# Optimization experiments

Hardware: AMD Instinct MI355X
Metric: run time of the kernel (lower is better)

## Reference

```python
import jax, jax.numpy as jnp
import numpy as np

B, N, C = 128, 197, 768
H = 12
HID = 3072
DROP = 0.1
EPS = 1e-5


def _layernorm(x, g, b):
    m = jnp.mean(x, axis=-1, keepdims=True)
    v = jnp.var(x, axis=-1, keepdims=True)
    return (x - m) * jax.lax.rsqrt(v + EPS) * g + b


def setup_inputs() -> dict:
    key = jax.random.key(0)
    ks = jax.random.split(key, 6)
    def lin(k, fan_in, fan_out):
        return (jax.random.normal(k, (fan_in, fan_out), jnp.float32) * (fan_in ** -0.5))
    return {
        "x": jax.random.normal(ks[0], (B, N, C), jnp.float32),
        "ln1_g": jnp.ones((C,), jnp.float32),
        "ln1_b": jnp.zeros((C,), jnp.float32),
        "Wqkv": lin(ks[1], C, 3 * C),          # qkv_bias=False
        "Wproj": lin(ks[2], C, C),
        "bproj": jnp.zeros((C,), jnp.float32),
        "ln2_g": jnp.ones((C,), jnp.float32),
        "ln2_b": jnp.zeros((C,), jnp.float32),
        "W1": lin(ks[3], C, HID),
        "b1": jnp.zeros((HID,), jnp.float32),
        "W2": lin(ks[4], HID, C),
        "b2": jnp.zeros((C,), jnp.float32),
    }


def reference(x, ln1_g, ln1_b, Wqkv, Wproj, bproj, ln2_g, ln2_b, W1, b1, W2, b2):
    Bx, Nx, Cx = x.shape
    hd = Cx // H
    thr = int((Nx - 1) * DROP)            # 19
    keep = (Nx - 1) - (thr + 1)           # 176 patches kept (rank > thr)

    # ---- drop_low_attn: unscaled q@k^T, mean over heads, cls->patch scores ----
    qkv = (x @ Wqkv).reshape(Bx, Nx, 3, H, hd).transpose(2, 0, 3, 1, 4)
    q, k = qkv[0], qkv[1]
    attn0 = jnp.einsum('bhnd,bhmd->bhnm', q, k)        # no scale, no softmax
    scores = jnp.mean(attn0, axis=1)[:, 0, 1:]          # [B, N-1]
    rank = jnp.argsort(jnp.argsort(scores, axis=1), axis=1)
    keep_mask = rank > thr                              # exactly `keep` True per row
    # indices of kept patches in original order (stable argsort of ~mask)
    idx = jnp.argsort((~keep_mask).astype(jnp.int32), axis=1)[:, :keep] + 1
    tok = jnp.concatenate([jnp.zeros((Bx, 1), idx.dtype), idx], axis=1)  # cls + kept
    x = jnp.take_along_axis(x, tok[:, :, None], axis=1) / (1.0 - DROP)   # [B, 177, C]
    Np = keep + 1

    # ---- attention block (scaled softmax attention) ----
    h = _layernorm(x, ln1_g, ln1_b)
    qkv2 = (h @ Wqkv).reshape(Bx, Np, 3, H, hd).transpose(2, 0, 3, 1, 4)
    q2, k2, v2 = qkv2[0], qkv2[1], qkv2[2]
    a = jax.nn.softmax(jnp.einsum('bhnd,bhmd->bhnm', q2, k2) * (hd ** -0.5), axis=-1)
    o = jnp.einsum('bhnm,bhmd->bhnd', a, v2).transpose(0, 2, 1, 3).reshape(Bx, Np, Cx)
    x = x + (o @ Wproj + bproj)

    # ---- MLP block ----
    h = _layernorm(x, ln2_g, ln2_b)
    x = x + (jax.nn.gelu(h @ W1 + b1, approximate=False) @ W2 + b2)
    return x
```

## Files before the change

kernel.cpp:

```cpp
#include <hip/hip_runtime.h>
#include <math.h>

#define BB 128
#define NTOK 197
#define CC 768
#define HH 12
#define HD 64
#define HIDN 3072
#define NP 177
#define NPATCH 196
#define THRK 19
#define MR (BB*NP)

using short8 = __attribute__((ext_vector_type(8))) short;
using f32x4  = __attribute__((ext_vector_type(4))) float;

__device__ __forceinline__ unsigned short f2b(float f){
  unsigned u = __builtin_bit_cast(unsigned, f);
  u += 0x7fffu + ((u >> 16) & 1u);
  return (unsigned short)(u >> 16);
}

__device__ __forceinline__ float fast_gelu(float v){
  float u = v * 0.70710678118654752f;
  float a = fabsf(u);
  float t = 1.0f / fmaf(0.3275911f, a, 1.0f);
  float p = fmaf(1.061405429f, t, -1.453152027f);
  p = fmaf(p, t, 1.421413741f);
  p = fmaf(p, t, -0.284496736f);
  p = fmaf(p, t, 0.254829592f);
  p = p * t;
  float e = __expf(-a*a);
  float erfu = copysignf(1.0f - p*e, u);
  return 0.5f * v * (1.0f + erfu);
}

__device__ __forceinline__ void gload16(const void* src, void* lds){
  __builtin_amdgcn_global_load_lds(
      (const __attribute__((address_space(1))) unsigned int*)src,
      (__attribute__((address_space(3))) unsigned int*)lds,
      16, 0, 0);
}

__global__ void tcvt_kernel(const float* __restrict__ in, unsigned short* __restrict__ out, int K, int N){
  __shared__ float tile[64][65];
  int n0 = blockIdx.x*64, k0 = blockIdx.y*64;
  int t = threadIdx.x;
  int r = t >> 6, c = t & 63;
  #pragma unroll
  for (int i = 0; i < 16; ++i)
    tile[r + i*4][c] = in[(size_t)(k0 + r + i*4)*N + n0 + c];
  __syncthreads();
  #pragma unroll
  for (int i = 0; i < 16; ++i)
    out[(size_t)(n0 + r + i*4)*K + k0 + c] = f2b(tile[c][r + i*4]);
}

__global__ void q0_kernel(const float* __restrict__ x, const float* __restrict__ Wqkv, float* __restrict__ q0){
  int b = blockIdx.x, t = threadIdx.x;
  int c = blockIdx.y*256 + t;
  __shared__ float xs[CC];
  for (int j = t; j < CC; j += 256) xs[j] = x[(size_t)b*NTOK*CC + j];
  __syncthreads();
  double acc = 0.0;
  for (int j = 0; j < CC; ++j) acc = fma((double)xs[j], (double)Wqkv[(size_t)j*(3*CC) + c], acc);
  q0[b*CC + c] = (float)acc;
}

__global__ void wvec_kernel(const float* __restrict__ Wqkv, const float* __restrict__ q0, float* __restrict__ wv){
  int b = blockIdx.x;
  int j = blockIdx.y*4 + (threadIdx.x >> 6);
  int l = threadIdx.x & 63;
  const float* row = Wqkv + (size_t)j*(3*CC) + CC;
  const float* qs = q0 + b*CC;
  double acc = 0.0;
  for (int c = l; c < CC; c += 64) acc = fma((double)row[c], (double)qs[c], acc);
  for (int off = 32; off; off >>= 1) acc += __shfl_down(acc, off);
  if (l == 0) wv[b*CC + j] = (float)acc;
}

__global__ void score_kernel(const float* __restrict__ x, const float* __restrict__ wv, float* __restrict__ sc){
  int m = blockIdx.x, b = blockIdx.y, l = threadIdx.x;
  const float* xr = x + ((size_t)b*NTOK + 1 + m)*CC;
  const float* wr = wv + b*CC;
  double acc = 0.0;
  for (int c = l; c < CC; c += 64) acc = fma((double)xr[c], (double)wr[c], acc);
  for (int off = 32; off; off >>= 1) acc += __shfl_down(acc, off);
  if (l == 0) sc[b*NPATCH + m] = (float)(acc * (1.0/12.0));
}

__global__ void select_kernel(const float* __restrict__ sc, int* __restrict__ tok){
  int b = blockIdx.x, t = threadIdx.x;
  __shared__ float s[NPATCH];
  __shared__ int kp[NPATCH];
  for (int m = t; m < NPATCH; m += 256) s[m] = sc[b*NPATCH + m];
  __syncthreads();
  for (int m = t; m < NPATCH; m += 256){
    float v = s[m]; int rank = 0;
    for (int j = 0; j < NPATCH; ++j){
      float u = s[j];
      rank += (u < v) || (u == v && j < m);
    }
    kp[m] = (rank > THRK) ? 1 : 0;
  }
  __syncthreads();
  for (int m = t; m < NPATCH; m += 256){
    if (kp[m]){
      int pos = 0;
      for (int j = 0; j < m; ++j) pos += kp[j];
      tok[b*NP + 1 + pos] = m + 1;
    }
  }
  if (t == 0) tok[b*NP] = 0;
}

__global__ void gather_kernel(const float* __restrict__ x, const int* __restrict__ tok, float* __restrict__ xk){
  int i = blockIdx.x, b = blockIdx.y, t = threadIdx.x;
  int src = tok[b*NP + i];
  const float* xr = x + ((size_t)b*NTOK + src)*CC;
  float* o = xk + ((size_t)b*NP + i)*CC;
  for (int c = t; c < CC; c += 256) o[c] = xr[c] * (1.0f/0.9f);
}

__global__ void ln_kernel(const float* __restrict__ in, const float* __restrict__ g,
                          const float* __restrict__ bt, unsigned short* __restrict__ out){
  int row = blockIdx.x, t = threadIdx.x;
  const float* xr = in + (size_t)row*CC;
  float v0 = xr[t], v1 = xr[t+256], v2 = xr[t+512];
  float s = v0+v1+v2, ss = v0*v0+v1*v1+v2*v2;
  for (int off = 32; off; off >>= 1){ s += __shfl_down(s, off); ss += __shfl_down(ss, off); }
  __shared__ float red[8];
  int wid = t >> 6, lane = t & 63;
  if (lane == 0){ red[wid] = s; red[4+wid] = ss; }
  __syncthreads();
  if (t == 0){
    float S = red[0]+red[1]+red[2]+red[3], SS = red[4]+red[5]+red[6]+red[7];
    float mean = S * (1.0f/CC);
    float var = SS * (1.0f/CC) - mean*mean;
    red[0] = mean; red[1] = rsqrtf(var + 1e-5f);
  }
  __syncthreads();
  float mean = red[0], rstd = red[1];
  unsigned short* orow = out + (size_t)row*CC;
  orow[t]     = f2b((v0-mean)*rstd*g[t]     + bt[t]);
  orow[t+256] = f2b((v1-mean)*rstd*g[t+256] + bt[t+256]);
  orow[t+512] = f2b((v2-mean)*rstd*g[t+512] + bt[t+512]);
}

template<int EPI>
__global__ __launch_bounds__(256) void gemm128(
    const unsigned short* __restrict__ A, const unsigned short* __restrict__ Bt,
    const float* __restrict__ bias, const float* __restrict__ res, void* __restrict__ outp,
    int M, int N, int K)
{
  __shared__ __align__(16) short As[2][128*32];
  __shared__ __align__(16) short Bs[2][128*32];
  int nwg = gridDim.x, o = blockIdx.x;
  int q = nwg >> 3, rr = nwg & 7;
  int xcd = o & 7, seq = o >> 3;
  int wg = (xcd < rr) ? xcd*(q+1) + seq : rr*(q+1) + (xcd - rr)*q + seq;
  int nx = N >> 7;
  int m0 = (wg / nx) << 7, n0 = (wg % nx) << 7;

  int t = threadIdx.x, w = t >> 6, l = t & 63;
  int wr = w >> 1, wc = w & 1;
  int srow = w*16 + (l >> 2);
  int sk8  = (l & 3)*8;
  const unsigned short* Abase = A  + (size_t)(m0 + srow)*K + sk8;
  const unsigned short* Bbase = Bt + (size_t)(n0 + srow)*K + sk8;
  f32x4 acc[4][4] = {};

  int nt = K >> 5;
  #pragma unroll
  for (int j = 0; j < 2; ++j){
    gload16(Abase + (size_t)(j*64)*K, &As[0][(j*64 + w*16)*32]);
    gload16(Bbase + (size_t)(j*64)*K, &Bs[0][(j*64 + w*16)*32]);
  }
  __syncthreads();

  int cur = 0;
  for (int ti = 0; ti < nt; ++ti){
    if (ti + 1 < nt){
      int kt = (ti + 1) << 5;
      #pragma unroll
      for (int j = 0; j < 2; ++j){
        gload16(Abase + (size_t)(j*64)*K + kt, &As[cur^1][(j*64 + w*16)*32]);
        gload16(Bbase + (size_t)(j*64)*K + kt, &Bs[cur^1][(j*64 + w*16)*32]);
      }
    }
    short8 af[4], bf[4];
    #pragma unroll
    for (int i = 0; i < 4; ++i){
      af[i] = *reinterpret_cast<const short8*>(&As[cur][(wr*64 + i*16 + (l&15))*32 + (l>>4)*8]);
      bf[i] = *reinterpret_cast<const short8*>(&Bs[cur][(wc*64 + i*16 + (l&15))*32 + (l>>4)*8]);
    }
    #pragma unroll
    for (int i = 0; i < 4; ++i)
      #pragma unroll
      for (int jn = 0; jn < 4; ++jn)
        acc[i][jn] = __builtin_amdgcn_mfma_f32_16x16x32_bf16(af[i], bf[jn], acc[i][jn], 0, 0, 0);
    __syncthreads();
    cur ^= 1;
  }

  #pragma unroll
  for (int i = 0; i < 4; ++i)
  #pragma unroll
  for (int jn = 0; jn < 4; ++jn){
    int row = m0 + wr*64 + i*16 + (l>>4)*4;
    int col = n0 + wc*64 + jn*16 + (l&15);
    #pragma unroll
    for (int r = 0; r < 4; ++r){
      float v = acc[i][jn][r];
      if (EPI != 0) v += bias[col];
      if (EPI == 2) v = fast_gelu(v);
      if (EPI == 1 || EPI == 3) v += res[(size_t)(row+r)*N + col];
      if (EPI == 0 || EPI == 2) ((unsigned short*)outp)[(size_t)(row+r)*N + col] = f2b(v);
      else                      ((float*)outp)[(size_t)(row+r)*N + col] = v;
    }
  }
}

__global__ __launch_bounds__(256) void attn_kernel(const unsigned short* __restrict__ qkv2,
                                                   unsigned short* __restrict__ o)
{
  int rt = blockIdx.x, h = blockIdx.y, b = blockIdx.z;
  int t = threadIdx.x, w = t >> 6, l = t & 63;
  __shared__ short Vt[64*192];
  __shared__ short P[4][16*192];
  for (int idx = t; idx < NP*8; idx += 256){
    int m = idx >> 3, d0 = (idx & 7)*8;
    short8 v = *reinterpret_cast<const short8*>(qkv2 + (size_t)(b*NP+m)*(3*CC) + 2*CC + h*HD + d0);
    #pragma unroll
    for (int j = 0; j < 8; ++j) Vt[(d0+j)*192 + m] = v[j];
  }
  for (int idx = t; idx < 64*15; idx += 256){
    int d = idx/15, m = NP + idx%15;
    Vt[d*192 + m] = 0;
  }
  __syncthreads();
  int nb = rt*64 + w*16;
  int g = l >> 4, c = l & 15;
  int nq = nb + c; if (nq > NP-1) nq = NP-1;
  const unsigned short* qrow = qkv2 + (size_t)(b*NP+nq)*(3*CC) + h*HD + 8*g;
  short8 aq0 = *reinterpret_cast<const short8*>(qrow);
  short8 aq1 = *reinterpret_cast<const short8*>(qrow + 32);
  f32x4 acc[12];
  #pragma unroll
  for (int ct = 0; ct < 12; ++ct){
    int m = ct*16 + c; if (m > NP-1) m = NP-1;
    const unsigned short* krow = qkv2 + (size_t)(b*NP+m)*(3*CC) + CC + h*HD + 8*g;
    short8 bk0 = *reinterpret_cast<const short8*>(krow);
    short8 bk1 = *reinterpret_cast<const short8*>(krow + 32);
    f32x4 a = {};
    a = __builtin_amdgcn_mfma_f32_16x16x32_bf16(aq0, bk0, a, 0, 0, 0);
    a = __builtin_amdgcn_mfma_f32_16x16x32_bf16(aq1, bk1, a, 0, 0, 0);
    acc[ct] = a;
  }
  float mx[4] = {-INFINITY, -INFINITY, -INFINITY, -INFINITY};
  #pragma unroll
  for (int ct = 0; ct < 12; ++ct){
    bool valid = (ct*16 + c) < NP;
    #pragma unroll
    for (int r = 0; r < 4; ++r){
      float v = valid ? acc[ct][r]*0.125f : -INFINITY;
      acc[ct][r] = v;
      mx[r] = fmaxf(mx[r], v);
    }
  }
  #pragma unroll
  for (int off = 1; off < 16; off <<= 1){
    #pragma unroll
    for (int r = 0; r < 4; ++r) mx[r] = fmaxf(mx[r], __shfl_xor(mx[r], off));
  }
  float sm2[4] = {0.f, 0.f, 0.f, 0.f};
  #pragma unroll
  for (int ct = 0; ct < 12; ++ct)
    #pragma unroll
    for (int r = 0; r < 4; ++r){
      float e = __expf(acc[ct][r] - mx[r]);
      acc[ct][r] = e; sm2[r] += e;
    }
  #pragma unroll
  for (int off = 1; off < 16; off <<= 1){
    #pragma unroll
    for (int r = 0; r < 4; ++r) sm2[r] += __shfl_xor(sm2[r], off);
  }
  float inv[4];
  #pragma unroll
  for (int r = 0; r < 4; ++r) inv[r] = 1.0f / sm2[r];
  #pragma unroll
  for (int ct = 0; ct < 12; ++ct)
    #pragma unroll
    for (int r = 0; r < 4; ++r)
      P[w][(4*g + r)*192 + ct*16 + c] = (short)f2b(acc[ct][r]*inv[r]);
  f32x4 acc2[4] = {};
  __builtin_amdgcn_s_setprio(1);
  #pragma unroll
  for (int ks = 0; ks < 6; ++ks){
    short8 pa = *reinterpret_cast<const short8*>(&P[w][c*192 + ks*32 + 8*g]);
    #pragma unroll
    for (int ct2 = 0; ct2 < 4; ++ct2){
      short8 bv = *reinterpret_cast<const short8*>(&Vt[(ct2*16 + c)*192 + ks*32 + 8*g]);
      acc2[ct2] = __builtin_amdgcn_mfma_f32_16x16x32_bf16(pa, bv, acc2[ct2], 0, 0, 0);
    }
  }
  __builtin_amdgcn_s_setprio(0);
  #pragma unroll
  for (int ct2 = 0; ct2 < 4; ++ct2){
    #pragma unroll
    for (int r = 0; r < 4; ++r){
      int n = nb + 4*g + r;
      if (n < NP) o[(size_t)(b*NP+n)*CC + h*HD + ct2*16 + c] = f2b(acc2[ct2][r]);
    }
  }
}

extern "C" void kernel_launch(void* const* d_in, const int* in_sizes, int n_in,
                              void* d_out, int out_size, void* d_ws, size_t ws_size,
                              hipStream_t stream) {
  const float* x     = (const float*)d_in[0];
  const float* ln1g  = (const float*)d_in[1];
  const float* ln1b  = (const float*)d_in[2];
  const float* Wqkv  = (const float*)d_in[3];
  const float* Wproj = (const float*)d_in[4];
  const float* bproj = (const float*)d_in[5];
  const float* ln2g  = (const float*)d_in[6];
  const float* ln2b  = (const float*)d_in[7];
  const float* W1    = (const float*)d_in[8];
  const float* b1    = (const float*)d_in[9];
  const float* W2    = (const float*)d_in[10];
  const float* b2    = (const float*)d_in[11];
  float* out = (float*)d_out;

  unsigned char* base = (unsigned char*)d_ws;
  size_t off = 0;
  auto alloc = [&](size_t bytes) -> void* {
    off = (off + 255) & ~(size_t)255;
    void* p = base + off;
    off += bytes;
    return p;
  };
  unsigned short* WqkvT  = (unsigned short*)alloc((size_t)(3*CC)*CC*2);
  unsigned short* WprojT = (unsigned short*)alloc((size_t)CC*CC*2);
  unsigned short* W1T    = (unsigned short*)alloc((size_t)HIDN*CC*2);
  unsigned short* W2T    = (unsigned short*)alloc((size_t)CC*HIDN*2);
  float* q0   = (float*)alloc((size_t)BB*CC*4);
  float* wv   = (float*)alloc((size_t)BB*CC*4);
  float* sc   = (float*)alloc((size_t)BB*NPATCH*4);
  int*   tok  = (int*)alloc((size_t)BB*NP*4);
  unsigned short* hbuf = (unsigned short*)alloc((size_t)MR*CC*2);
  float* xk   = (float*)alloc((size_t)MR*CC*4);
  unsigned short* qkv2 = (unsigned short*)alloc((size_t)MR*3*CC*2);
  if (off > ws_size) return;

  unsigned short* obuf = hbuf;
  unsigned short* mid  = (unsigned short*)xk;
  float* x2 = out;

  tcvt_kernel<<<dim3((3*CC)/64, CC/64), 256, 0, stream>>>(Wqkv,  WqkvT,  CC, 3*CC);
  tcvt_kernel<<<dim3(CC/64, CC/64),     256, 0, stream>>>(Wproj, WprojT, CC, CC);
  tcvt_kernel<<<dim3(HIDN/64, CC/64),   256, 0, stream>>>(W1,    W1T,    CC, HIDN);
  tcvt_kernel<<<dim3(CC/64, HIDN/64),   256, 0, stream>>>(W2,    W2T,    HIDN, CC);

  q0_kernel<<<dim3(BB, 3), 256, 0, stream>>>(x, Wqkv, q0);
  wvec_kernel<<<dim3(BB, CC/4), 256, 0, stream>>>(Wqkv, q0, wv);
  score_kernel<<<dim3(NPATCH, BB), 64, 0, stream>>>(x, wv, sc);
  select_kernel<<<BB, 256, 0, stream>>>(sc, tok);
  gather_kernel<<<dim3(NP, BB), 256, 0, stream>>>(x, tok, xk);

  ln_kernel<<<MR, 256, 0, stream>>>(xk, ln1g, ln1b, hbuf);
  gemm128<0><<<(MR/128)*((3*CC)/128), 256, 0, stream>>>(hbuf, WqkvT, nullptr, nullptr, qkv2, MR, 3*CC, CC);
  attn_kernel<<<dim3(3, HH, BB), 256, 0, stream>>>(qkv2, obuf);
  gemm128<1><<<(MR/128)*(CC/128), 256, 0, stream>>>(obuf, WprojT, bproj, xk, x2, MR, CC, CC);

  ln_kernel<<<MR, 256, 0, stream>>>(x2, ln2g, ln2b, hbuf);
  gemm128<2><<<(MR/128)*(HIDN/128), 256, 0, stream>>>(hbuf, W1T, b1, nullptr, mid, MR, HIDN, CC);
  gemm128<3><<<(MR/128)*(CC/128), 256, 0, stream>>>(mid, W2T, b2, x2, out, MR, CC, HIDN);
}
```

Baseline: 844.1 us.

## Triple-buffer GEMM LDS with swizzled layout and prefetch distance two

Replaces the double-buffered A/B shared tiles in the bf16 MFMA GEMM with a three-stage ring that prefetches two k-tiles ahead. It uses explicit vmcnt waits and raw barriers instead of __syncthreads. Global-to-LDS copies and fragment reads use an XOR swizzle on the 8-element chunk index, intended to cut LDS bank conflicts. MFMA blocks are wrapped in s_setprio, and launch bounds request 3 blocks per CU. The cost is 48KB of LDS per block and a loop that assumes the k-tile count is a multiple of three.

Result: faster. 767.2 us (-9.1%).

```diff
diff --git a/kernel.cpp b/kernel.cpp
--- a/kernel.cpp
+++ b/kernel.cpp
@@ -148,13 +148,12 @@
 }
 
 template<int EPI>
-__global__ __launch_bounds__(256) void gemm128(
+__global__ __launch_bounds__(256, 3) void gemm128(
     const unsigned short* __restrict__ A, const unsigned short* __restrict__ Bt,
     const float* __restrict__ bias, const float* __restrict__ res, void* __restrict__ outp,
     int M, int N, int K)
 {
-  __shared__ __align__(16) short As[2][128*32];
-  __shared__ __align__(16) short Bs[2][128*32];
+  __shared__ __align__(16) short lds[3*8192];
   int nwg = gridDim.x, o = blockIdx.x;
   int q = nwg >> 3, rr = nwg & 7;
   int xcd = o & 7, seq = o >> 3;
@@ -164,43 +163,59 @@
 
   int t = threadIdx.x, w = t >> 6, l = t & 63;
   int wr = w >> 1, wc = w & 1;
-  int srow = w*16 + (l >> 2);
-  int sk8  = (l & 3)*8;
-  const unsigned short* Abase = A  + (size_t)(m0 + srow)*K + sk8;
-  const unsigned short* Bbase = Bt + (size_t)(n0 + srow)*K + sk8;
   f32x4 acc[4][4] = {};
-
   int nt = K >> 5;
-  #pragma unroll
-  for (int j = 0; j < 2; ++j){
-    gload16(Abase + (size_t)(j*64)*K, &As[0][(j*64 + w*16)*32]);
-    gload16(Bbase + (size_t)(j*64)*K, &Bs[0][(j*64 + w*16)*32]);
-  }
-  __syncthreads();
-
-  int cur = 0;
-  for (int ti = 0; ti < nt; ++ti){
-    if (ti + 1 < nt){
-      int kt = (ti + 1) << 5;
-      #pragma unroll
-      for (int j = 0; j < 2; ++j){
-        gload16(Abase + (size_t)(j*64)*K + kt, &As[cur^1][(j*64 + w*16)*32]);
-        gload16(Bbase + (size_t)(j*64)*K + kt, &Bs[cur^1][(j*64 + w*16)*32]);
-      }
-    }
+
+  auto stage = [&](int kti, int sb){
+    int kt = kti << 5;
+    short* buf = &lds[sb*8192];
+    #pragma unroll
+    for (int j = 0; j < 2; ++j){
+      int row = j*64 + w*16 + (l >> 2);
+      int gk = ((l & 3) ^ ((row >> 1) & 3)) * 8;
+      gload16(A  + (size_t)(m0 + row)*K + kt + gk, &buf[(j*64 + w*16)*32]);
+      gload16(Bt + (size_t)(n0 + row)*K + kt + gk, &buf[4096 + (j*64 + w*16)*32]);
+    }
+  };
+  auto compute = [&](int cb){
+    const short* Ab = &lds[cb*8192];
+    const short* Bb = Ab + 4096;
     short8 af[4], bf[4];
     #pragma unroll
     for (int i = 0; i < 4; ++i){
-      af[i] = *reinterpret_cast<const short8*>(&As[cur][(wr*64 + i*16 + (l&15))*32 + (l>>4)*8]);
-      bf[i] = *reinterpret_cast<const short8*>(&Bs[cur][(wc*64 + i*16 + (l&15))*32 + (l>>4)*8]);
-    }
+      int Ra = wr*64 + i*16 + (l & 15);
+      af[i] = *reinterpret_cast<const short8*>(&Ab[Ra*32 + (((l>>4) ^ ((Ra>>1)&3)))*8]);
+      int Rb = wc*64 + i*16 + (l & 15);
+      bf[i] = *reinterpret_cast<const short8*>(&Bb[Rb*32 + (((l>>4) ^ ((Rb>>1)&3)))*8]);
+    }
+    __builtin_amdgcn_s_setprio(1);
     #pragma unroll
     for (int i = 0; i < 4; ++i)
       #pragma unroll
       for (int jn = 0; jn < 4; ++jn)
         acc[i][jn] = __builtin_amdgcn_mfma_f32_16x16x32_bf16(af[i], bf[jn], acc[i][jn], 0, 0, 0);
-    __syncthreads();
-    cur ^= 1;
+    __builtin_amdgcn_s_setprio(0);
+  };
+  auto step = [&](int ti, int cb, int sb){
+    bool more = (ti + 2) < nt;
+    if (more) stage(ti + 2, sb);
+    compute(cb);
+    if (more) asm volatile("s_waitcnt vmcnt(4)" ::: "memory");
+    else      asm volatile("s_waitcnt vmcnt(0)" ::: "memory");
+    __builtin_amdgcn_s_barrier();
+    asm volatile("" ::: "memory");
+  };
+
+  stage(0, 0); stage(1, 1);
+  asm volatile("s_waitcnt vmcnt(4)" ::: "memory");
+  __builtin_amdgcn_s_barrier();
+  asm volatile("" ::: "memory");
+
+  #pragma unroll 1
+  for (int ti = 0; ti < nt; ti += 3){
+    step(ti,     0, 2);
+    step(ti + 1, 1, 0);
+    step(ti + 2, 2, 1);
   }
 
   #pragma unroll
```
